# Kernel optimization log

Hardware: AMD Instinct MI355X
Metric: run time of the kernel (lower is better)

The kernel has to match this reference:

```python
import jax, jax.numpy as jnp
import numpy as np

D_MODEL, D_K, H = 1024, 64, 16
B, S = 2, 2048

def setup_inputs() -> dict:
    key = jax.random.key(0)
    ks = jax.random.split(key, 9)
    s_in = 1.0 / np.sqrt(D_MODEL)
    x = jax.random.normal(ks[0], (B, S, D_MODEL), dtype=jnp.float32)
    Wq = jax.random.uniform(ks[1], (H, D_MODEL, D_K), jnp.float32, -s_in, s_in)
    bq = jax.random.uniform(ks[2], (H, D_K), jnp.float32, -s_in, s_in)
    Wk = jax.random.uniform(ks[3], (H, D_MODEL, D_K), jnp.float32, -s_in, s_in)
    bk = jax.random.uniform(ks[4], (H, D_K), jnp.float32, -s_in, s_in)
    Wv = jax.random.uniform(ks[5], (H, D_MODEL, D_K), jnp.float32, -s_in, s_in)
    bv = jax.random.uniform(ks[6], (H, D_K), jnp.float32, -s_in, s_in)
    Wo = jax.random.uniform(ks[7], (D_MODEL, D_MODEL), jnp.float32, -s_in, s_in)
    bo = jax.random.uniform(ks[8], (D_MODEL,), jnp.float32, -s_in, s_in)
    return {"x": x, "Wq": Wq, "bq": bq, "Wk": Wk, "bk": bk,
            "Wv": Wv, "bv": bv, "Wo": Wo, "bo": bo}

def reference(x, Wq, bq, Wk, bk, Wv, bv, Wo, bo):
    # PositionLinear = Linear + ReLU (the ReLU is part of the original math)
    Q = jax.nn.relu(jnp.einsum('bsd,hdk->bhsk', x, Wq) + bq[:, None, :])
    K = jax.nn.relu(jnp.einsum('bsd,hdk->bhsk', x, Wk) + bk[:, None, :])
    V = jax.nn.relu(jnp.einsum('bsd,hdk->bhsk', x, Wv) + bv[:, None, :])
    scale = jnp.sqrt(jnp.float32(Q.shape[-1]))
    scores = jnp.einsum('bhsk,bhtk->bhst', Q, K) / scale  # [B,H,S,S]
    attn = jax.nn.softmax(scores, axis=-1)
    ctx = jnp.einsum('bhst,bhtk->bhsk', attn, V)
    # concat heads along feature dim (head order matches torch.cat(output, 2))
    ctx = jnp.transpose(ctx, (0, 2, 1, 3)).reshape(x.shape[0], x.shape[1], -1)
    out = jax.nn.relu(ctx @ Wo + bo)
    return out
```

## Files before the change

### kernel.cpp

```cpp
#include <hip/hip_runtime.h>
#include <cstddef>

#define D_MODEL 1024
#define DK 64
#define NH 16
#define NB 2
#define SEQ 2048

typedef __attribute__((ext_vector_type(8))) short bf16x8;
typedef __attribute__((ext_vector_type(4))) float floatx4;

static __device__ __forceinline__ unsigned short f2bf(float f) {
    union { float f; unsigned u; } v; v.f = f;
    unsigned r = (v.u + 0x7fffu + ((v.u >> 16) & 1u)) >> 16;
    return (unsigned short)r;
}

static __device__ __forceinline__ unsigned pk2bf(float lo, float hi) {
    unsigned ua = __float_as_uint(lo) + 0x8000u;
    unsigned ub = __float_as_uint(hi) + 0x8000u;
    return __builtin_amdgcn_perm(ub, ua, 0x07060302u);
}

static __device__ __forceinline__ float swz16(float x) {
    return __int_as_float(__builtin_amdgcn_ds_swizzle(__float_as_int(x), 0x401F));
}

static __device__ __forceinline__ void gld16(const unsigned short* g, unsigned short* l) {
    __builtin_amdgcn_global_load_lds(
        (const __attribute__((address_space(1))) unsigned int*)g,
        (__attribute__((address_space(3))) unsigned int*)l, 16, 0, 0);
}

__global__ __launch_bounds__(256) void convert_x(const float* __restrict__ x,
                                                 unsigned short* __restrict__ xb)
{
    const size_t i = ((size_t)blockIdx.x * 256 + threadIdx.x) * 16;
#pragma unroll
    for (int c = 0; c < 16; c += 4) {
        float4 v = *(const float4*)&x[i + c];
        uint2 pk;
        pk.x = (unsigned)f2bf(v.x) | ((unsigned)f2bf(v.y) << 16);
        pk.y = (unsigned)f2bf(v.z) | ((unsigned)f2bf(v.w) << 16);
        *(uint2*)&xb[i + c] = pk;
    }
}

__global__ __launch_bounds__(256) void pack_w(
    const float* __restrict__ Wq, const float* __restrict__ Wk,
    const float* __restrict__ Wv, const float* __restrict__ Wo,
    unsigned short* __restrict__ Bqkv, unsigned short* __restrict__ Bo)
{
    __shared__ float T[64][65];
    const int t   = blockIdx.x;
    const int tid = threadIdx.x;
    const int rr   = tid >> 2;
    const int cseg = (tid & 3) * 16;

    const float* src;
    unsigned short* dst;
    if (t < 768) {
        const int proj = t / 256, rem = t % 256;
        const int h = rem >> 4, d0 = (rem & 15) * 64;
        const float* W = proj == 0 ? Wq : (proj == 1 ? Wk : Wv);
        src = W + ((size_t)h * 1024 + d0) * 64;
#pragma unroll
        for (int c = 0; c < 16; c += 4) {
            float4 v = *(const float4*)&src[(size_t)rr * 64 + cseg + c];
            T[rr][cseg + c + 0] = v.x; T[rr][cseg + c + 1] = v.y;
            T[rr][cseg + c + 2] = v.z; T[rr][cseg + c + 3] = v.w;
        }
        __syncthreads();
        dst = &Bqkv[((size_t)proj * 1024 + h * 64 + rr) * 1024 + d0 + cseg];
    } else {
        const int t2 = t - 768;
        const int k0 = (t2 >> 4) * 64, nb0 = (t2 & 15) * 64;
#pragma unroll
        for (int c = 0; c < 16; c += 4) {
            float4 v = *(const float4*)&Wo[(size_t)(k0 + rr) * 1024 + nb0 + cseg + c];
            T[rr][cseg + c + 0] = v.x; T[rr][cseg + c + 1] = v.y;
            T[rr][cseg + c + 2] = v.z; T[rr][cseg + c + 3] = v.w;
        }
        __syncthreads();
        dst = &Bo[(size_t)(nb0 + rr) * 1024 + k0 + cseg];
    }
    unsigned int w[8];
#pragma unroll
    for (int ii = 0; ii < 8; ii++) {
        unsigned short lo = f2bf(T[cseg + ii * 2 + 0][rr]);
        unsigned short hi = f2bf(T[cseg + ii * 2 + 1][rr]);
        w[ii] = (unsigned)lo | ((unsigned)hi << 16);
    }
    *(uint4*)(dst + 0) = make_uint4(w[0], w[1], w[2], w[3]);
    *(uint4*)(dst + 8) = make_uint4(w[4], w[5], w[6], w[7]);
}

__global__ __launch_bounds__(256) void gemm_qkv(
    const unsigned short* __restrict__ Abf,
    const unsigned short* __restrict__ Bp,
    const float* __restrict__ bq, const float* __restrict__ bk,
    const float* __restrict__ bv,
    unsigned short* __restrict__ Qo, unsigned short* __restrict__ Ko,
    unsigned short* __restrict__ Vo)
{
    __shared__ __align__(16) unsigned short As[128 * 32];
    __shared__ __align__(16) unsigned short Bs[128 * 32];

    const int tid  = threadIdx.x;
    const int wv   = tid >> 6, lane = tid & 63;
    const int m0   = blockIdx.x * 128;
    const int n0   = blockIdx.y * 128;
    const int lq   = lane & 15, g = lane >> 4;
    const int wm   = (wv >> 1) * 64;
    const int wn   = (wv & 1) * 64;
    const int srow = lane >> 2;
    const int sseg = (lane & 3) * 8;

    floatx4 acc[4][4];
#pragma unroll
    for (int i = 0; i < 4; i++)
#pragma unroll
        for (int j = 0; j < 4; j++) acc[i][j] = (floatx4){0.f, 0.f, 0.f, 0.f};

    for (int k0 = 0; k0 < 1024; k0 += 32) {
#pragma unroll
        for (int r = 0; r < 2; r++) {
            const int chunk = wv * 2 + r;
            const int row   = chunk * 16 + srow;
            gld16(&Abf[(size_t)(m0 + row) * 1024 + k0 + sseg], &As[chunk * 512]);
            gld16(&Bp [(size_t)(n0 + row) * 1024 + k0 + sseg], &Bs[chunk * 512]);
        }
        __syncthreads();
        bf16x8 af[4], bfv[4];
#pragma unroll
        for (int i = 0; i < 4; i++)
            af[i] = *(const bf16x8*)&As[(wm + i * 16 + lq) * 32 + g * 8];
#pragma unroll
        for (int j = 0; j < 4; j++)
            bfv[j] = *(const bf16x8*)&Bs[(wn + j * 16 + lq) * 32 + g * 8];
#pragma unroll
        for (int i = 0; i < 4; i++)
#pragma unroll
            for (int j = 0; j < 4; j++)
                acc[i][j] = __builtin_amdgcn_mfma_f32_16x16x32_bf16(af[i], bfv[j], acc[i][j], 0, 0, 0);
        __syncthreads();
    }

    const int proj = n0 >> 10;
    const float* bias = proj == 0 ? bq : (proj == 1 ? bk : bv);
    unsigned short* OutQK = proj == 0 ? Qo : Ko;

#pragma unroll
    for (int j = 0; j < 4; j++) {
        const int n  = n0 + wn + j * 16 + lq;
        const int nn = n & 1023;
        const int h  = nn >> 6, dk = nn & 63;
        const float bb = bias[nn];
#pragma unroll
        for (int i = 0; i < 4; i++) {
            const int mbase = m0 + wm + i * 16 + g * 4;
            const int b_ = mbase >> 11;
            const int s_ = mbase & (SEQ - 1);
            const int bh = b_ * NH + h;
            if (proj < 2) {
                const size_t fb = (((size_t)bh * 128 + (s_ >> 4)) * 2 + (dk >> 5)) * 512
                                + (size_t)((((dk & 31) >> 3) * 16) + (s_ & 15)) * 8 + (dk & 7);
#pragma unroll
                for (int r = 0; r < 4; r++)
                    OutQK[fb + (size_t)r * 8] = f2bf(fmaxf(acc[i][j][r] + bb, 0.f));
            } else {
                const size_t fb = ((((size_t)bh * 32 + (s_ >> 6)) * 4 + (dk >> 4)) * 2
                                   + ((s_ >> 5) & 1)) * 512
                                + (size_t)((((s_ & 31) >> 3) * 16) + (dk & 15)) * 8 + (s_ & 7);
                uint2 pk;
                pk.x = (unsigned)f2bf(fmaxf(acc[i][j][0] + bb, 0.f))
                     | ((unsigned)f2bf(fmaxf(acc[i][j][1] + bb, 0.f)) << 16);
                pk.y = (unsigned)f2bf(fmaxf(acc[i][j][2] + bb, 0.f))
                     | ((unsigned)f2bf(fmaxf(acc[i][j][3] + bb, 0.f)) << 16);
                *(uint2*)&Vo[fb] = pk;
            }
        }
    }
}

__global__ __launch_bounds__(256, 2) void attn_kernel(
    const unsigned short* __restrict__ Qf,
    const unsigned short* __restrict__ Kf,
    const unsigned short* __restrict__ Vf,
    unsigned short* __restrict__ ctxb)
{
    __shared__ __align__(16) unsigned short KVs[2][8192];
    __shared__ __align__(16) unsigned short Ps[4][4][16][40];
    __shared__ float Lx[2][4][64];

    const int blk = blockIdx.x;
    const int xcd = blk & 7;
    const int j_  = blk >> 3;
    const int bh  = xcd * 4 + (j_ & 3);
    const int qt  = j_ >> 2;

    const int tid  = threadIdx.x;
    const int wv   = tid >> 6;
    const int lane = tid & 63;
    const int lq   = lane & 15;
    const int g    = lane >> 4;
    const int qh   = wv >> 1;
    const int kh   = wv & 1;

    const int q0 = qt * 128 + qh * 64;

    bf16x8 qa[4], qb[4];
    const size_t qfB = ((size_t)bh * 128 + (q0 >> 4)) * 1024 + (size_t)lane * 8;
#pragma unroll
    for (int t = 0; t < 4; t++) {
        qa[t] = *(const bf16x8*)&Qf[qfB + (size_t)t * 1024];
        qb[t] = *(const bf16x8*)&Qf[qfB + (size_t)t * 1024 + 512];
    }

    const float C  = 0.18033688011112042f;
    const float MC = 2.8853900817779267f;

    const unsigned short* KtB = &Kf[(size_t)bh * 131072];
    const unsigned short* VtB = &Vf[(size_t)bh * 131072];

    float l[4] = {0.f, 0.f, 0.f, 0.f};
    floatx4 acc[4][4];
#pragma unroll
    for (int t = 0; t < 4; t++)
#pragma unroll
        for (int n = 0; n < 4; n++) acc[t][n] = (floatx4){0.f, 0.f, 0.f, 0.f};

#pragma unroll
    for (int r = 0; r < 2; r++) {
        const int c = wv * 2 + r;
        gld16(&KtB[(size_t)c * 512 + lane * 8], &KVs[0][c * 512]);
        gld16(&VtB[(size_t)c * 512 + lane * 8], &KVs[0][4096 + c * 512]);
    }
    __syncthreads();

    for (int jt = 0; jt < SEQ / 64; jt++) {
        const int buf = jt & 1;

        const int jn = (jt + 1) & (SEQ / 64 - 1);
        const unsigned short* ktn = &KtB[(size_t)jn * 4096];
        const unsigned short* vtn = &VtB[(size_t)jn * 4096];
#pragma unroll
        for (int r = 0; r < 2; r++) {
            const int c = wv * 2 + r;
            gld16(&ktn[(size_t)c * 512 + lane * 8], &KVs[buf ^ 1][c * 512]);
            gld16(&vtn[(size_t)c * 512 + lane * 8], &KVs[buf ^ 1][4096 + c * 512]);
        }

        const unsigned short* kb = &KVs[buf][0];
        const unsigned short* vb = &KVs[buf][4096];

        bf16x8 k0a = *(const bf16x8*)&kb[(2 * kh + 0) * 1024 + lane * 8];
        bf16x8 k0b = *(const bf16x8*)&kb[(2 * kh + 0) * 1024 + 512 + lane * 8];
        bf16x8 k1a = *(const bf16x8*)&kb[(2 * kh + 1) * 1024 + lane * 8];
        bf16x8 k1b = *(const bf16x8*)&kb[(2 * kh + 1) * 1024 + 512 + lane * 8];

        bf16x8 vr[4];
#pragma unroll
        for (int n = 0; n < 4; n++)
            vr[n] = *(const bf16x8*)&vb[(n * 2 + kh) * 512 + lane * 8];

#pragma unroll
        for (int t = 0; t < 4; t++) {
            floatx4 s0 = (floatx4){0.f, 0.f, 0.f, 0.f};
            s0 = __builtin_amdgcn_mfma_f32_16x16x32_bf16(k0a, qa[t], s0, 0, 0, 0);
            s0 = __builtin_amdgcn_mfma_f32_16x16x32_bf16(k0b, qb[t], s0, 0, 0, 0);
            floatx4 s1 = (floatx4){0.f, 0.f, 0.f, 0.f};
            s1 = __builtin_amdgcn_mfma_f32_16x16x32_bf16(k1a, qa[t], s1, 0, 0, 0);
            s1 = __builtin_amdgcn_mfma_f32_16x16x32_bf16(k1b, qb[t], s1, 0, 0, 0);

            float p00 = __builtin_amdgcn_exp2f(fmaf(s0[0], C, -MC));
            float p01 = __builtin_amdgcn_exp2f(fmaf(s0[1], C, -MC));
            float p02 = __builtin_amdgcn_exp2f(fmaf(s0[2], C, -MC));
            float p03 = __builtin_amdgcn_exp2f(fmaf(s0[3], C, -MC));
            l[t] += (p00 + p01) + (p02 + p03);
            uint2 pk0;
            pk0.x = pk2bf(p00, p01);
            pk0.y = pk2bf(p02, p03);
            *(uint2*)&Ps[wv][t][lq][g * 4] = pk0;

            float p10 = __builtin_amdgcn_exp2f(fmaf(s1[0], C, -MC));
            float p11 = __builtin_amdgcn_exp2f(fmaf(s1[1], C, -MC));
            float p12 = __builtin_amdgcn_exp2f(fmaf(s1[2], C, -MC));
            float p13 = __builtin_amdgcn_exp2f(fmaf(s1[3], C, -MC));
            l[t] += (p10 + p11) + (p12 + p13);
            uint2 pk1;
            pk1.x = pk2bf(p10, p11);
            pk1.y = pk2bf(p12, p13);
            *(uint2*)&Ps[wv][t][lq][16 + g * 4] = pk1;
        }
        __builtin_amdgcn_s_waitcnt(0xC07F);

        bf16x8 pb[4];
#pragma unroll
        for (int t = 0; t < 4; t++)
            pb[t] = *(const bf16x8*)&Ps[wv][t][lq][g * 8];

#pragma unroll
        for (int t = 0; t < 4; t++)
#pragma unroll
            for (int n = 0; n < 4; n++)
                acc[t][n] = __builtin_amdgcn_mfma_f32_16x16x32_bf16(vr[n], pb[t], acc[t][n], 0, 0, 0);

        __syncthreads();
    }

#pragma unroll
    for (int t = 0; t < 4; t++) {
        l[t] += swz16(l[t]);
        l[t] += __shfl_xor(l[t], 32, 64);
    }

    float* red = (float*)&KVs[0][0] + (size_t)qh * 4096;
    if (kh == 1) {
#pragma unroll
        for (int t = 0; t < 4; t++) {
#pragma unroll
            for (int n = 0; n < 4; n++)
                *(floatx4*)&red[(t * 4 + n) * 256 + lane * 4] = acc[t][n];
            Lx[qh][t][lane] = l[t];
        }
    }
    __syncthreads();
    if (kh == 0) {
        const int b_ = bh >> 4, h_ = bh & 15;
#pragma unroll
        for (int t = 0; t < 4; t++) {
            const float lt = l[t] + Lx[qh][t][lane];
            const float li = 1.f / lt;
#pragma unroll
            for (int n = 0; n < 4; n++) {
                floatx4 a = acc[t][n];
                floatx4 b = *(const floatx4*)&red[(t * 4 + n) * 256 + lane * 4];
                uint2 pk;
                pk.x = pk2bf((a[0] + b[0]) * li, (a[1] + b[1]) * li);
                pk.y = pk2bf((a[2] + b[2]) * li, (a[3] + b[3]) * li);
                *(uint2*)&ctxb[((size_t)(b_ * SEQ) + q0 + t * 16 + lq) * D_MODEL
                               + h_ * DK + n * 16 + g * 4] = pk;
            }
        }
    }
}

__global__ __launch_bounds__(256) void gemm_o(
    const unsigned short* __restrict__ Abf,
    const unsigned short* __restrict__ Bp,
    const float* __restrict__ bo,
    float* __restrict__ out)
{
    __shared__ __align__(16) unsigned short As[128 * 32];
    __shared__ __align__(16) unsigned short Bs[128 * 32];

    const int tid  = threadIdx.x;
    const int wv   = tid >> 6, lane = tid & 63;
    const int m0   = blockIdx.x * 128;
    const int n0   = blockIdx.y * 128;
    const int lq   = lane & 15, g = lane >> 4;
    const int wm   = (wv >> 1) * 64;
    const int wn   = (wv & 1) * 64;
    const int srow = lane >> 2;
    const int sseg = (lane & 3) * 8;

    floatx4 acc[4][4];
#pragma unroll
    for (int i = 0; i < 4; i++)
#pragma unroll
        for (int j = 0; j < 4; j++) acc[i][j] = (floatx4){0.f, 0.f, 0.f, 0.f};

    for (int k0 = 0; k0 < 1024; k0 += 32) {
#pragma unroll
        for (int r = 0; r < 2; r++) {
            const int chunk = wv * 2 + r;
            const int row   = chunk * 16 + srow;
            gld16(&Abf[(size_t)(m0 + row) * 1024 + k0 + sseg], &As[chunk * 512]);
            gld16(&Bp [(size_t)(n0 + row) * 1024 + k0 + sseg], &Bs[chunk * 512]);
        }
        __syncthreads();
        bf16x8 af[4], bfv[4];
#pragma unroll
        for (int i = 0; i < 4; i++)
            af[i] = *(const bf16x8*)&As[(wm + i * 16 + lq) * 32 + g * 8];
#pragma unroll
        for (int j = 0; j < 4; j++)
            bfv[j] = *(const bf16x8*)&Bs[(wn + j * 16 + lq) * 32 + g * 8];
#pragma unroll
        for (int i = 0; i < 4; i++)
#pragma unroll
            for (int j = 0; j < 4; j++)
                acc[i][j] = __builtin_amdgcn_mfma_f32_16x16x32_bf16(af[i], bfv[j], acc[i][j], 0, 0, 0);
        __syncthreads();
    }

#pragma unroll
    for (int j = 0; j < 4; j++) {
        const int n  = n0 + wn + j * 16 + lq;
        const float bb = bo[n];
#pragma unroll
        for (int i = 0; i < 4; i++) {
#pragma unroll
            for (int r = 0; r < 4; r++) {
                const int m = m0 + wm + i * 16 + g * 4 + r;
                out[(size_t)m * 1024 + n] = fmaxf(acc[i][j][r] + bb, 0.f);
            }
        }
    }
}

extern "C" void kernel_launch(void* const* d_in, const int* in_sizes, int n_in,
                              void* d_out, int out_size, void* d_ws, size_t ws_size,
                              hipStream_t stream) {
    const float* x  = (const float*)d_in[0];
    const float* Wq = (const float*)d_in[1];
    const float* bq = (const float*)d_in[2];
    const float* Wk = (const float*)d_in[3];
    const float* bk = (const float*)d_in[4];
    const float* Wv = (const float*)d_in[5];
    const float* bv = (const float*)d_in[6];
    const float* Wo = (const float*)d_in[7];
    const float* bo = (const float*)d_in[8];
    float* out = (float*)d_out;

    const size_t perE = (size_t)NB * NH * SEQ * DK;
    unsigned short* xbf  = (unsigned short*)d_ws;
    unsigned short* Bqkv = xbf  + (size_t)4096 * 1024;
    unsigned short* Bo   = Bqkv + (size_t)3072 * 1024;
    unsigned short* Qfr  = Bo   + (size_t)1024 * 1024;
    unsigned short* Kfr  = Qfr + perE;
    unsigned short* Vfr  = Kfr + perE;
    unsigned short* Cbf  = Vfr + perE;

    convert_x<<<1024, 256, 0, stream>>>(x, xbf);
    pack_w<<<1024, 256, 0, stream>>>(Wq, Wk, Wv, Wo, Bqkv, Bo);
    gemm_qkv<<<dim3(32, 24), 256, 0, stream>>>(xbf, Bqkv, bq, bk, bv, Qfr, Kfr, Vfr);
    attn_kernel<<<512, 256, 0, stream>>>(Qfr, Kfr, Vfr, Cbf);
    gemm_o<<<dim3(32, 8), 256, 0, stream>>>(Cbf, Bo, bo, out);
}
```

Baseline: 193.5 us.

## Restructure attention block to 8 waves with 128-key tiles and 32-query slices

The attention kernel moves from 256 to 512 threads per block. Each wave pair now handles 32 queries instead of 64, and the key/value tile loaded per iteration grows from 64 to 128 keys, which halves the number of loop iterations and barriers. The P round-trip through LDS now happens per 16-query subtile, with a smaller per-wave scratch area. Per-wave register pressure goes down, allowing higher occupancy (launch bounds 512,4), at the cost of more LDS per block and finer-grained waitcnt stalls between the exp and PV phases.

Measured after the change: 196.9 us. About the same (+1.8%).

```diff
diff --git a/kernel.cpp b/kernel.cpp
--- a/kernel.cpp
+++ b/kernel.cpp
@@ -183,15 +183,15 @@
     }
 }
 
-__global__ __launch_bounds__(256, 2) void attn_kernel(
+__global__ __launch_bounds__(512, 4) void attn_kernel(
     const unsigned short* __restrict__ Qf,
     const unsigned short* __restrict__ Kf,
     const unsigned short* __restrict__ Vf,
     unsigned short* __restrict__ ctxb)
 {
-    __shared__ __align__(16) unsigned short KVs[2][8192];
-    __shared__ __align__(16) unsigned short Ps[4][4][16][40];
-    __shared__ float Lx[2][4][64];
+    __shared__ __align__(16) unsigned short KVs[2][16384];
+    __shared__ __align__(16) unsigned short Ps[8][16][40];
+    __shared__ float Lx[4][2][64];
 
     const int blk = blockIdx.x;
     const int xcd = blk & 7;
@@ -204,15 +204,15 @@
     const int lane = tid & 63;
     const int lq   = lane & 15;
     const int g    = lane >> 4;
-    const int qh   = wv >> 1;
+    const int qq   = wv >> 1;
     const int kh   = wv & 1;
 
-    const int q0 = qt * 128 + qh * 64;
-
-    bf16x8 qa[4], qb[4];
+    const int q0 = qt * 128 + qq * 32;
+
+    bf16x8 qa[2], qb[2];
     const size_t qfB = ((size_t)bh * 128 + (q0 >> 4)) * 1024 + (size_t)lane * 8;
 #pragma unroll
-    for (int t = 0; t < 4; t++) {
+    for (int t = 0; t < 2; t++) {
         qa[t] = *(const bf16x8*)&Qf[qfB + (size_t)t * 1024];
         qb[t] = *(const bf16x8*)&Qf[qfB + (size_t)t * 1024 + 512];
     }
@@ -223,10 +223,10 @@
     const unsigned short* KtB = &Kf[(size_t)bh * 131072];
     const unsigned short* VtB = &Vf[(size_t)bh * 131072];
 
-    float l[4] = {0.f, 0.f, 0.f, 0.f};
-    floatx4 acc[4][4];
-#pragma unroll
-    for (int t = 0; t < 4; t++)
+    float l[2] = {0.f, 0.f};
+    floatx4 acc[2][4];
+#pragma unroll
+    for (int t = 0; t < 2; t++)
 #pragma unroll
         for (int n = 0; n < 4; n++) acc[t][n] = (floatx4){0.f, 0.f, 0.f, 0.f};
 
@@ -234,103 +234,101 @@
     for (int r = 0; r < 2; r++) {
         const int c = wv * 2 + r;
         gld16(&KtB[(size_t)c * 512 + lane * 8], &KVs[0][c * 512]);
-        gld16(&VtB[(size_t)c * 512 + lane * 8], &KVs[0][4096 + c * 512]);
+        gld16(&VtB[(size_t)c * 512 + lane * 8], &KVs[0][8192 + c * 512]);
     }
     __syncthreads();
 
-    for (int jt = 0; jt < SEQ / 64; jt++) {
+    for (int jt = 0; jt < SEQ / 128; jt++) {
         const int buf = jt & 1;
 
-        const int jn = (jt + 1) & (SEQ / 64 - 1);
-        const unsigned short* ktn = &KtB[(size_t)jn * 4096];
-        const unsigned short* vtn = &VtB[(size_t)jn * 4096];
+        const int jn = (jt + 1) & (SEQ / 128 - 1);
+        const unsigned short* ktn = &KtB[(size_t)jn * 8192];
+        const unsigned short* vtn = &VtB[(size_t)jn * 8192];
 #pragma unroll
         for (int r = 0; r < 2; r++) {
             const int c = wv * 2 + r;
             gld16(&ktn[(size_t)c * 512 + lane * 8], &KVs[buf ^ 1][c * 512]);
-            gld16(&vtn[(size_t)c * 512 + lane * 8], &KVs[buf ^ 1][4096 + c * 512]);
+            gld16(&vtn[(size_t)c * 512 + lane * 8], &KVs[buf ^ 1][8192 + c * 512]);
         }
 
         const unsigned short* kb = &KVs[buf][0];
-        const unsigned short* vb = &KVs[buf][4096];
-
-        bf16x8 k0a = *(const bf16x8*)&kb[(2 * kh + 0) * 1024 + lane * 8];
-        bf16x8 k0b = *(const bf16x8*)&kb[(2 * kh + 0) * 1024 + 512 + lane * 8];
-        bf16x8 k1a = *(const bf16x8*)&kb[(2 * kh + 1) * 1024 + lane * 8];
-        bf16x8 k1b = *(const bf16x8*)&kb[(2 * kh + 1) * 1024 + 512 + lane * 8];
-
-        bf16x8 vr[4];
-#pragma unroll
-        for (int n = 0; n < 4; n++)
-            vr[n] = *(const bf16x8*)&vb[(n * 2 + kh) * 512 + lane * 8];
-
-#pragma unroll
-        for (int t = 0; t < 4; t++) {
-            floatx4 s0 = (floatx4){0.f, 0.f, 0.f, 0.f};
-            s0 = __builtin_amdgcn_mfma_f32_16x16x32_bf16(k0a, qa[t], s0, 0, 0, 0);
-            s0 = __builtin_amdgcn_mfma_f32_16x16x32_bf16(k0b, qb[t], s0, 0, 0, 0);
-            floatx4 s1 = (floatx4){0.f, 0.f, 0.f, 0.f};
-            s1 = __builtin_amdgcn_mfma_f32_16x16x32_bf16(k1a, qa[t], s1, 0, 0, 0);
-            s1 = __builtin_amdgcn_mfma_f32_16x16x32_bf16(k1b, qb[t], s1, 0, 0, 0);
-
-            float p00 = __builtin_amdgcn_exp2f(fmaf(s0[0], C, -MC));
-            float p01 = __builtin_amdgcn_exp2f(fmaf(s0[1], C, -MC));
-            float p02 = __builtin_amdgcn_exp2f(fmaf(s0[2], C, -MC));
-            float p03 = __builtin_amdgcn_exp2f(fmaf(s0[3], C, -MC));
-            l[t] += (p00 + p01) + (p02 + p03);
-            uint2 pk0;
-            pk0.x = pk2bf(p00, p01);
-            pk0.y = pk2bf(p02, p03);
-            *(uint2*)&Ps[wv][t][lq][g * 4] = pk0;
-
-            float p10 = __builtin_amdgcn_exp2f(fmaf(s1[0], C, -MC));
-            float p11 = __builtin_amdgcn_exp2f(fmaf(s1[1], C, -MC));
-            float p12 = __builtin_amdgcn_exp2f(fmaf(s1[2], C, -MC));
-            float p13 = __builtin_amdgcn_exp2f(fmaf(s1[3], C, -MC));
-            l[t] += (p10 + p11) + (p12 + p13);
-            uint2 pk1;
-            pk1.x = pk2bf(p10, p11);
-            pk1.y = pk2bf(p12, p13);
-            *(uint2*)&Ps[wv][t][lq][16 + g * 4] = pk1;
-        }
-        __builtin_amdgcn_s_waitcnt(0xC07F);
-
-        bf16x8 pb[4];
-#pragma unroll
-        for (int t = 0; t < 4; t++)
-            pb[t] = *(const bf16x8*)&Ps[wv][t][lq][g * 8];
-
-#pragma unroll
-        for (int t = 0; t < 4; t++)
+        const unsigned short* vb = &KVs[buf][8192];
+
+#pragma unroll
+        for (int s = 0; s < 2; s++) {
+            const int kg = 4 * kh + 2 * s;
+            bf16x8 a0 = *(const bf16x8*)&kb[(kg + 0) * 1024 + lane * 8];
+            bf16x8 a1 = *(const bf16x8*)&kb[(kg + 0) * 1024 + 512 + lane * 8];
+            bf16x8 a2 = *(const bf16x8*)&kb[(kg + 1) * 1024 + lane * 8];
+            bf16x8 a3 = *(const bf16x8*)&kb[(kg + 1) * 1024 + 512 + lane * 8];
+            bf16x8 vr[4];
 #pragma unroll
             for (int n = 0; n < 4; n++)
-                acc[t][n] = __builtin_amdgcn_mfma_f32_16x16x32_bf16(vr[n], pb[t], acc[t][n], 0, 0, 0);
-
-        __syncthreads();
-    }
-
-#pragma unroll
-    for (int t = 0; t < 4; t++) {
+                vr[n] = *(const bf16x8*)&vb[(kh * 4 + n) * 1024 + s * 512 + lane * 8];
+
+#pragma unroll
+            for (int t = 0; t < 2; t++) {
+                floatx4 s0 = (floatx4){0.f, 0.f, 0.f, 0.f};
+                s0 = __builtin_amdgcn_mfma_f32_16x16x32_bf16(a0, qa[t], s0, 0, 0, 0);
+                s0 = __builtin_amdgcn_mfma_f32_16x16x32_bf16(a1, qb[t], s0, 0, 0, 0);
+                floatx4 s1 = (floatx4){0.f, 0.f, 0.f, 0.f};
+                s1 = __builtin_amdgcn_mfma_f32_16x16x32_bf16(a2, qa[t], s1, 0, 0, 0);
+                s1 = __builtin_amdgcn_mfma_f32_16x16x32_bf16(a3, qb[t], s1, 0, 0, 0);
+
+                float p00 = __builtin_amdgcn_exp2f(fmaf(s0[0], C, -MC));
+                float p01 = __builtin_amdgcn_exp2f(fmaf(s0[1], C, -MC));
+                float p02 = __builtin_amdgcn_exp2f(fmaf(s0[2], C, -MC));
+                float p03 = __builtin_amdgcn_exp2f(fmaf(s0[3], C, -MC));
+                l[t] += (p00 + p01) + (p02 + p03);
+                uint2 pk0;
+                pk0.x = pk2bf(p00, p01);
+                pk0.y = pk2bf(p02, p03);
+                *(uint2*)&Ps[wv][lq][g * 4] = pk0;
+
+                float p10 = __builtin_amdgcn_exp2f(fmaf(s1[0], C, -MC));
+                float p11 = __builtin_amdgcn_exp2f(fmaf(s1[1], C, -MC));
+                float p12 = __builtin_amdgcn_exp2f(fmaf(s1[2], C, -MC));
+                float p13 = __builtin_amdgcn_exp2f(fmaf(s1[3], C, -MC));
+                l[t] += (p10 + p11) + (p12 + p13);
+                uint2 pk1;
+                pk1.x = pk2bf(p10, p11);
+                pk1.y = pk2bf(p12, p13);
+                *(uint2*)&Ps[wv][lq][16 + g * 4] = pk1;
+
+                __builtin_amdgcn_s_waitcnt(0xC07F);
+                bf16x8 pb = *(const bf16x8*)&Ps[wv][lq][g * 8];
+
+#pragma unroll
+                for (int n = 0; n < 4; n++)
+                    acc[t][n] = __builtin_amdgcn_mfma_f32_16x16x32_bf16(vr[n], pb, acc[t][n], 0, 0, 0);
+            }
+        }
+
+        __syncthreads();
+    }
+
+#pragma unroll
+    for (int t = 0; t < 2; t++) {
         l[t] += swz16(l[t]);
         l[t] += __shfl_xor(l[t], 32, 64);
     }
 
-    float* red = (float*)&KVs[0][0] + (size_t)qh * 4096;
+    float* red = (float*)&KVs[0][0] + (size_t)qq * 2048;
     if (kh == 1) {
 #pragma unroll
-        for (int t = 0; t < 4; t++) {
+        for (int t = 0; t < 2; t++) {
+            Lx[qq][t][lane] = l[t];
 #pragma unroll
             for (int n = 0; n < 4; n++)
                 *(floatx4*)&red[(t * 4 + n) * 256 + lane * 4] = acc[t][n];
-            Lx[qh][t][lane] = l[t];
         }
     }
     __syncthreads();
     if (kh == 0) {
         const int b_ = bh >> 4, h_ = bh & 15;
 #pragma unroll
-        for (int t = 0; t < 4; t++) {
-            const float lt = l[t] + Lx[qh][t][lane];
+        for (int t = 0; t < 2; t++) {
+            const float lt = l[t] + Lx[qq][t][lane];
             const float li = 1.f / lt;
 #pragma unroll
             for (int n = 0; n < 4; n++) {
@@ -436,6 +434,6 @@
     convert_x<<<1024, 256, 0, stream>>>(x, xbf);
     pack_w<<<1024, 256, 0, stream>>>(Wq, Wk, Wv, Wo, Bqkv, Bo);
     gemm_qkv<<<dim3(32, 24), 256, 0, stream>>>(xbf, Bqkv, bq, bk, bv, Qfr, Kfr, Vfr);
-    attn_kernel<<<512, 256, 0, stream>>>(Qfr, Kfr, Vfr, Cbf);
+    attn_kernel<<<512, 512, 0, stream>>>(Qfr, Kfr, Vfr, Cbf);
     gemm_o<<<dim3(32, 8), 256, 0, stream>>>(Cbf, Bo, bo, out);
 }
```
